# Kernel optimization log

Measured on AMD Instinct MI355X. Metric: run time of the kernel, lower is better.

The kernel has to match this reference:

```python
import jax, jax.numpy as jnp
import numpy as np
from jax import lax

B, CIN, H, W = 32, 256, 28, 28
COUT, KS, KEXP = 256, 3, 4
HIDDEN = int(CIN * 0.25)  # ratio hard-coded to 0.25 in the module


def setup_inputs() -> dict:
    key = jax.random.key(0)
    k1, k2, k3, k4 = jax.random.split(key, 4)
    x = jax.random.normal(k1, (B, CIN, H, W), dtype=jnp.float32)
    # SE (InvertedEx) params: fc1 (1x1 conv, no bias), fc2 (1x1 conv, bias)
    fc1_w = jax.random.normal(k2, (HIDDEN, CIN), dtype=jnp.float32) * np.float32(np.sqrt(2.0 / CIN))
    fc2_w = jax.random.normal(k3, (KEXP * COUT, HIDDEN), dtype=jnp.float32) * np.float32(np.sqrt(2.0 / HIDDEN))
    fc2_b = jnp.zeros((KEXP * COUT,), dtype=jnp.float32)
    # K expert conv kernels, he_std = sqrt(2) * (CIN*KS^2)^-0.5
    he_std = np.float32(np.sqrt(2.0) * (CIN * KS * KS) ** -0.5)
    weight = jax.random.normal(k4, (KEXP, COUT, CIN, KS, KS), dtype=jnp.float32) * he_std
    return {"x": x, "fc1_w": fc1_w, "fc2_w": fc2_w, "fc2_b": fc2_b, "weight": weight}


def reference(x, fc1_w, fc2_w, fc2_b, weight):
    # --- SE routing ---
    pooled = jnp.mean(x, axis=(2, 3))                        # [B, CIN]
    h = jax.nn.relu(pooled @ fc1_w.T)                        # [B, HIDDEN]
    y = (h @ fc2_w.T + fc2_b).reshape(B, KEXP, COUT)         # [B, K, COUT]
    prob = jax.nn.softmax(y / jnp.sqrt(jnp.float32(HIDDEN)), axis=1)  # softmax over K
    # --- aggregate per-sample kernels ---
    agg_w = jnp.einsum('bko,koihw->boihw', prob, weight)     # [B, COUT, CIN, KS, KS]
    # --- per-sample conv (batched implicit GEMM via vmap) ---
    def conv1(xi, wi):
        return lax.conv_general_dilated(
            xi[None], wi, window_strides=(1, 1), padding=((1, 1), (1, 1)),
            dimension_numbers=('NCHW', 'OIHW', 'NCHW'))[0]
    out = jax.vmap(conv1)(x, agg_w)                          # [B, COUT, H, W]
    return out
```

## Files before the change

### kernel.cpp

```cpp
#include <hip/hip_runtime.h>
#include <math.h>

#define B_    32
#define CIN_  256
#define HW_   784
#define H_    28
#define W_    28
#define COUT_ 256
#define KEXP_ 4
#define HID_  64

typedef short short8 __attribute__((ext_vector_type(8)));
typedef unsigned short ushort4v __attribute__((ext_vector_type(4)));
typedef float floatx16 __attribute__((ext_vector_type(16)));

__device__ __forceinline__ unsigned short f2bf(float f) {
    union { float f; unsigned int u; } v; v.f = f;
    unsigned int r = (v.u + 0x7FFFu + ((v.u >> 16) & 1u)) >> 16;
    return (unsigned short)r;
}

__global__ __launch_bounds__(256) void xpose_pool_kernel(const float* __restrict__ x,
                                                         unsigned short* __restrict__ x_t,
                                                         float* __restrict__ partial) {
    __shared__ float tile[32][33];
    int bid = blockIdx.x;
    int b   = bid / 200;
    int rem = bid - b * 200;
    int icg = rem / 25;
    int pxt = rem % 25;
    int ic0 = icg * 32;
    int px0 = pxt * 32;
    int t = threadIdx.x;
    int c = t & 31, rr = t >> 5;
    #pragma unroll
    for (int r = 0; r < 4; ++r) {
        int icr = rr + r * 8;
        int px = px0 + c;
        float v = (px < HW_) ? x[((size_t)(b * CIN_ + ic0 + icr)) * HW_ + px] : 0.f;
        tile[icr][c] = v;
    }
    __syncthreads();
    #pragma unroll
    for (int r = 0; r < 4; ++r) {
        int pxr = rr + r * 8;
        int px = px0 + pxr;
        if (px < HW_)
            x_t[((size_t)b * HW_ + px) * CIN_ + ic0 + c] = f2bf(tile[c][pxr]);
    }
    if (t < 32) {
        float s = 0.f;
        #pragma unroll
        for (int cc = 0; cc < 32; ++cc) s += tile[t][cc];
        partial[((size_t)b * 25 + pxt) * CIN_ + ic0 + t] = s * (1.0f / HW_);
    }
}

__global__ __launch_bounds__(256) void pool_kernel(const float* __restrict__ x,
                                                   float* __restrict__ pooled) {
    int w = blockIdx.x * 4 + (threadIdx.x >> 6);
    int lane = threadIdx.x & 63;
    const float* p = x + (size_t)w * HW_;
    float s = 0.f;
    for (int i = lane; i < HW_; i += 64) s += p[i];
    for (int off = 32; off; off >>= 1) s += __shfl_down(s, off);
    if (lane == 0) pooled[w] = s * (1.0f / HW_);
}

__global__ __launch_bounds__(256) void se3_kernel(const float* __restrict__ partial,
                                                  const float* __restrict__ fc1_w,
                                                  const float* __restrict__ fc2_w,
                                                  const float* __restrict__ fc2_b,
                                                  float* __restrict__ prob) {
    __shared__ float pl[CIN_];
    __shared__ float h[HID_];
    __shared__ float wb[16640];
    int b = blockIdx.x, t = threadIdx.x;
    {
        float s = 0.f;
        for (int pt = 0; pt < 25; ++pt)
            s += partial[((size_t)b * 25 + pt) * CIN_ + t];
        pl[t] = s;
    }
    #pragma unroll
    for (int i = 0; i < 16; ++i) {
        int l = t + i * 256;
        float4 v = *(const float4*)(fc1_w + (size_t)l * 4);
        int r = l >> 6, cc = (l & 63) * 4;
        float* dst = &wb[r * 257 + cc];
        dst[0] = v.x; dst[1] = v.y; dst[2] = v.z; dst[3] = v.w;
    }
    __syncthreads();
    if (t < HID_) {
        float s = 0.f;
        const float* wr = &wb[t * 257];
        for (int c = 0; c < CIN_; ++c) s += pl[c] * wr[c];
        h[t] = fmaxf(s, 0.f);
    }
    float yk[KEXP_];
    for (int k = 0; k < KEXP_; ++k) {
        __syncthreads();
        #pragma unroll
        for (int i = 0; i < 16; ++i) {
            int l = t + i * 256;
            float4 v = *(const float4*)(fc2_w + (size_t)k * COUT_ * HID_ + (size_t)l * 4);
            int o = l >> 4, jj = (l & 15) * 4;
            float* dst = &wb[o * 65 + jj];
            dst[0] = v.x; dst[1] = v.y; dst[2] = v.z; dst[3] = v.w;
        }
        __syncthreads();
        float s = fc2_b[k * COUT_ + t];
        const float* wr = &wb[t * 65];
        #pragma unroll
        for (int j = 0; j < HID_; ++j) s += h[j] * wr[j];
        yk[k] = s * 0.125f;
    }
    float m = yk[0];
    for (int k = 1; k < KEXP_; ++k) m = fmaxf(m, yk[k]);
    float e[KEXP_], sum = 0.f;
    for (int k = 0; k < KEXP_; ++k) { e[k] = expf(yk[k] - m); sum += e[k]; }
    float inv = 1.0f / sum;
    for (int k = 0; k < KEXP_; ++k)
        prob[b * (KEXP_ * COUT_) + k * COUT_ + t] = e[k] * inv;
}

__global__ __launch_bounds__(256) void se2_kernel(const float* __restrict__ pooled,
                                                  const float* __restrict__ fc1_w,
                                                  const float* __restrict__ fc2_w,
                                                  const float* __restrict__ fc2_b,
                                                  float* __restrict__ prob) {
    __shared__ float pl[CIN_];
    __shared__ float h[HID_];
    __shared__ float wb[16640];
    int b = blockIdx.x, t = threadIdx.x;
    pl[t] = pooled[b * CIN_ + t];
    #pragma unroll
    for (int i = 0; i < 16; ++i) {
        int l = t + i * 256;
        float4 v = *(const float4*)(fc1_w + (size_t)l * 4);
        int r = l >> 6, cc = (l & 63) * 4;
        float* dst = &wb[r * 257 + cc];
        dst[0] = v.x; dst[1] = v.y; dst[2] = v.z; dst[3] = v.w;
    }
    __syncthreads();
    if (t < HID_) {
        float s = 0.f;
        const float* wr = &wb[t * 257];
        for (int c = 0; c < CIN_; ++c) s += pl[c] * wr[c];
        h[t] = fmaxf(s, 0.f);
    }
    float yk[KEXP_];
    for (int k = 0; k < KEXP_; ++k) {
        __syncthreads();
        #pragma unroll
        for (int i = 0; i < 16; ++i) {
            int l = t + i * 256;
            float4 v = *(const float4*)(fc2_w + (size_t)k * COUT_ * HID_ + (size_t)l * 4);
            int o = l >> 4, jj = (l & 15) * 4;
            float* dst = &wb[o * 65 + jj];
            dst[0] = v.x; dst[1] = v.y; dst[2] = v.z; dst[3] = v.w;
        }
        __syncthreads();
        float s = fc2_b[k * COUT_ + t];
        const float* wr = &wb[t * 65];
        #pragma unroll
        for (int j = 0; j < HID_; ++j) s += h[j] * wr[j];
        yk[k] = s * 0.125f;
    }
    float m = yk[0];
    for (int k = 1; k < KEXP_; ++k) m = fmaxf(m, yk[k]);
    float e[KEXP_], sum = 0.f;
    for (int k = 0; k < KEXP_; ++k) { e[k] = expf(yk[k] - m); sum += e[k]; }
    float inv = 1.0f / sum;
    for (int k = 0; k < KEXP_; ++k)
        prob[b * (KEXP_ * COUT_) + k * COUT_ + t] = e[k] * inv;
}

__global__ __launch_bounds__(256) void agg3_kernel(const float* __restrict__ weight,
                                                   const float* __restrict__ prob,
                                                   unsigned short* __restrict__ agg) {
    __shared__ float ws_w[KEXP_ * CIN_ * 9];
    __shared__ float pb[KEXP_][8];
    int bid = blockIdx.x;
    int oc = bid & 255;
    int b0 = (bid >> 8) * 8;
    int t = threadIdx.x;
    #pragma unroll
    for (int i = 0; i < 9; ++i) {
        int e4 = t + i * 256;
        int k = e4 / 576;
        int r4 = e4 - k * 576;
        float4 v = *(const float4*)(weight + (size_t)k * 589824 + (size_t)oc * 2304 + (size_t)r4 * 4);
        *(float4*)&ws_w[e4 * 4] = v;
    }
    if (t < KEXP_ * 8) {
        int k = t >> 3, bb = t & 7;
        pb[k][bb] = prob[(size_t)(b0 + bb) * (KEXP_ * COUT_) + k * COUT_ + oc];
    }
    __syncthreads();
    int icg = t & 63, blane = t >> 6;
    for (int rs = 0; rs < 9; ++rs) {
        float wv[4][4];
        #pragma unroll
        for (int q = 0; q < 4; ++q)
            #pragma unroll
            for (int k = 0; k < 4; ++k)
                wv[q][k] = ws_w[k * 2304 + (icg * 4 + q) * 9 + rs];
        #pragma unroll
        for (int bb = 0; bb < 2; ++bb) {
            int bidx = blane * 2 + bb;
            float p0 = pb[0][bidx], p1 = pb[1][bidx], p2 = pb[2][bidx], p3 = pb[3][bidx];
            ushort4v pack;
            #pragma unroll
            for (int q = 0; q < 4; ++q) {
                float s = p0 * wv[q][0] + p1 * wv[q][1] + p2 * wv[q][2] + p3 * wv[q][3];
                pack[q] = f2bf(s);
            }
            *(ushort4v*)(agg + ((((size_t)(b0 + bidx) * 9 + rs) * COUT_ + oc)) * CIN_ + icg * 4) = pack;
        }
    }
}

__global__ __launch_bounds__(256, 1) void conv_mfma3_kernel(const unsigned short* __restrict__ x_t,
                                                            const unsigned short* __restrict__ agg,
                                                            float* __restrict__ out) {
    __shared__ __align__(16) short Xs[2][9 * 35 * 72];

    int gid = blockIdx.x;
    int b      = gid & 31;
    int oc0    = ((gid >> 5) & 1) * 128;
    int rowblk = gid >> 6;
    int py0 = rowblk * 7;

    int t = threadIdx.x;
    int lane = t & 63, w = t >> 6;
    int ml = lane & 31, kh = lane >> 5;

    floatx16 acc[7];
    #pragma unroll
    for (int j = 0; j < 7; ++j)
        #pragma unroll
        for (int r = 0; r < 16; ++r) acc[j][r] = 0.f;

    const unsigned short* xtb = x_t + (size_t)b * HW_ * CIN_;
    const unsigned short* aln = agg + (((size_t)b * 9 * COUT_) + oc0 + w * 32 + ml) * CIN_ + kh * 8;

    {
        #pragma unroll
        for (int i = 0; i < 10; ++i) {
            int l = t + i * 256;
            if (l < 2520) {
                int pos = l >> 3, g = l & 7;
                int row = pos / 35, col = pos - row * 35;
                int gy = py0 - 1 + row, gx = col - 1;
                short8 v = (short8)0;
                if ((unsigned)gy < 28u && (unsigned)gx < 28u)
                    v = *(const short8*)(xtb + ((size_t)(gy * W_ + gx)) * CIN_ + g * 8);
                *(short8*)&Xs[0][pos * 72 + g * 8] = v;
            }
        }
    }

    short8 Acur0, Acur1, Acur2, Anext0, Anext1, Anext2;
    Acur0 = *(const short8*)(aln + (size_t)(0 * 3 + 0) * (COUT_ * CIN_));
    Acur1 = *(const short8*)(aln + (size_t)(1 * 3 + 0) * (COUT_ * CIN_));
    Acur2 = *(const short8*)(aln + (size_t)(2 * 3 + 0) * (COUT_ * CIN_));
    int dxn = 1, kkn = 0, icn = 0;

    __syncthreads();

    for (int c = 0; c < 4; ++c) {
        int ic0 = c * 64;
        const short* xb = &Xs[c & 1][0];

        short8 Xl[10];
        if (c < 3) {
            #pragma unroll
            for (int i = 0; i < 10; ++i) {
                int l = t + i * 256;
                short8 v = (short8)0;
                if (l < 2520) {
                    int pos = l >> 3, g = l & 7;
                    int row = pos / 35, col = pos - row * 35;
                    int gy = py0 - 1 + row, gx = col - 1;
                    if ((unsigned)gy < 28u && (unsigned)gx < 28u)
                        v = *(const short8*)(xtb + ((size_t)(gy * W_ + gx)) * CIN_ + ic0 + 64 + g * 8);
                }
                Xl[i] = v;
            }
        }

        for (int kk = 0; kk < 4; ++kk) {
            for (int dx = 0; dx < 3; ++dx) {
                if (icn < 256) {
                    const unsigned short* ap = aln + icn + kkn * 16;
                    Anext0 = *(const short8*)(ap + (size_t)(0 * 3 + dxn) * (COUT_ * CIN_));
                    Anext1 = *(const short8*)(ap + (size_t)(1 * 3 + dxn) * (COUT_ * CIN_));
                    Anext2 = *(const short8*)(ap + (size_t)(2 * 3 + dxn) * (COUT_ * CIN_));
                    ++dxn;
                    if (dxn == 3) { dxn = 0; ++kkn; if (kkn == 4) { kkn = 0; icn += 64; } }
                }
                int va = (ml + dx) * 72 + kk * 16 + kh * 8;
                #pragma unroll
                for (int r = 0; r < 9; ++r) {
                    short8 Bf = *(const short8*)&xb[r * 2520 + va];
                    if (r <= 6)
                        acc[r]     = __builtin_amdgcn_mfma_f32_32x32x16_bf16(Acur0, Bf, acc[r], 0, 0, 0);
                    if (r >= 1 && r - 1 <= 6)
                        acc[r - 1] = __builtin_amdgcn_mfma_f32_32x32x16_bf16(Acur1, Bf, acc[r - 1], 0, 0, 0);
                    if (r >= 2)
                        acc[r - 2] = __builtin_amdgcn_mfma_f32_32x32x16_bf16(Acur2, Bf, acc[r - 2], 0, 0, 0);
                }
                Acur0 = Anext0; Acur1 = Anext1; Acur2 = Anext2;
            }
        }

        if (c < 3) {
            short* dstb = &Xs[(c & 1) ^ 1][0];
            #pragma unroll
            for (int i = 0; i < 10; ++i) {
                int l = t + i * 256;
                if (l < 2520) {
                    int pos = l >> 3, g = l & 7;
                    *(short8*)&dstb[pos * 72 + g * 8] = Xl[i];
                }
            }
        }
        __syncthreads();
    }

    if (ml < W_) {
        #pragma unroll
        for (int j = 0; j < 7; ++j) {
            float* op = out + ((size_t)(b * COUT_ + oc0 + w * 32)) * HW_ + (py0 + j) * W_ + ml;
            #pragma unroll
            for (int r = 0; r < 16; ++r) {
                int ocd = (r & 3) + 8 * (r >> 2) + 4 * kh;
                op[(size_t)ocd * HW_] = acc[j][r];
            }
        }
    }
}

__global__ __launch_bounds__(256) void conv_kernel(const float* __restrict__ x,
                                                   const float* __restrict__ weight,
                                                   const float* __restrict__ prob,
                                                   float* __restrict__ out) {
    __shared__ float xs[30 * 30];
    __shared__ float wagg[8][32][12];
    __shared__ float pl[KEXP_][8];

    int b  = blockIdx.x >> 5;
    int o0 = (blockIdx.x & 31) * 8;
    int t  = threadIdx.x;

    if (t < 32) {
        int k = t >> 3, oc = t & 7;
        pl[k][oc] = prob[b * (KEXP_ * COUT_) + k * COUT_ + o0 + oc];
    }
    int p0 = t;
    int pr[4], pc[4];
    bool pv[4];
    #pragma unroll
    for (int j = 0; j < 4; ++j) {
        int p = p0 + j * 256;
        pv[j] = p < HW_;
        pr[j] = p / W_;
        pc[j] = p % W_;
    }
    float acc[8][4];
    #pragma unroll
    for (int oc = 0; oc < 8; ++oc)
        #pragma unroll
        for (int j = 0; j < 4; ++j) acc[oc][j] = 0.f;

    int aoc = t >> 5, aii = t & 31;

    for (int ic0 = 0; ic0 < CIN_; ic0 += 32) {
        __syncthreads();
        {
            float w9[9];
            #pragma unroll
            for (int j = 0; j < 9; ++j) w9[j] = 0.f;
            int i = ic0 + aii;
            #pragma unroll
            for (int k = 0; k < KEXP_; ++k) {
                float pk = pl[k][aoc];
                const float* wp = weight + ((size_t)(k * COUT_ + o0 + aoc) * CIN_ + i) * 9;
                #pragma unroll
                for (int j = 0; j < 9; ++j) w9[j] += pk * wp[j];
            }
            #pragma unroll
            for (int j = 0; j < 9; ++j) wagg[aoc][aii][j] = w9[j];
        }
        for (int ii = 0; ii < 32; ++ii) {
            int i = ic0 + ii;
            __syncthreads();
            const float* xp = x + (size_t)(b * CIN_ + i) * HW_;
            for (int e = t; e < 900; e += 256) {
                int ry = e / 30, cx = e - ry * 30;
                int gy = ry - 1, gx = cx - 1;
                float v = 0.f;
                if ((unsigned)gy < 28u && (unsigned)gx < 28u) v = xp[gy * W_ + gx];
                xs[e] = v;
            }
            __syncthreads();
            float xv[4][9];
            #pragma unroll
            for (int j = 0; j < 4; ++j) {
                if (pv[j]) {
                    const float* xr = &xs[pr[j] * 30 + pc[j]];
                    xv[j][0] = xr[0];  xv[j][1] = xr[1];  xv[j][2] = xr[2];
                    xv[j][3] = xr[30]; xv[j][4] = xr[31]; xv[j][5] = xr[32];
                    xv[j][6] = xr[60]; xv[j][7] = xr[61]; xv[j][8] = xr[62];
                } else {
                    #pragma unroll
                    for (int q = 0; q < 9; ++q) xv[j][q] = 0.f;
                }
            }
            #pragma unroll
            for (int oc = 0; oc < 8; ++oc) {
                float4 wa = *(const float4*)&wagg[oc][ii][0];
                float4 wb2 = *(const float4*)&wagg[oc][ii][4];
                float  wc = wagg[oc][ii][8];
                #pragma unroll
                for (int j = 0; j < 4; ++j) {
                    acc[oc][j] += xv[j][0] * wa.x + xv[j][1] * wa.y + xv[j][2] * wa.z
                                + xv[j][3] * wa.w + xv[j][4] * wb2.x + xv[j][5] * wb2.y
                                + xv[j][6] * wb2.z + xv[j][7] * wb2.w + xv[j][8] * wc;
                }
            }
        }
    }
    #pragma unroll
    for (int oc = 0; oc < 8; ++oc) {
        float* op = out + (size_t)(b * COUT_ + o0 + oc) * HW_ + p0;
        #pragma unroll
        for (int j = 0; j < 4; ++j)
            if (pv[j]) op[j * 256] = acc[oc][j];
    }
}

extern "C" void kernel_launch(void* const* d_in, const int* in_sizes, int n_in,
                              void* d_out, int out_size, void* d_ws, size_t ws_size,
                              hipStream_t stream) {
    const float* x     = (const float*)d_in[0];
    const float* fc1_w = (const float*)d_in[1];
    const float* fc2_w = (const float*)d_in[2];
    const float* fc2_b = (const float*)d_in[3];
    const float* weight= (const float*)d_in[4];
    float* out = (float*)d_out;

    char* ws = (char*)d_ws;
    float* prob = (float*)(ws);
    unsigned short* x_t = (unsigned short*)(ws + 131072);
    unsigned short* agg = (unsigned short*)(ws + 12976128);
    float* partial = (float*)(ws + 12976128);
    const size_t WS_NEED = 12976128 + (size_t)B_ * 9 * COUT_ * CIN_ * 2;

    if (ws_size >= WS_NEED) {
        xpose_pool_kernel<<<B_ * 8 * 25, 256, 0, stream>>>(x, x_t, partial);
        se3_kernel<<<B_, 256, 0, stream>>>(partial, fc1_w, fc2_w, fc2_b, prob);
        agg3_kernel<<<4 * COUT_, 256, 0, stream>>>(weight, prob, agg);
        conv_mfma3_kernel<<<256, 256, 0, stream>>>(x_t, agg, out);
    } else {
        float* pooled = (float*)(ws + 131072);
        pool_kernel<<<(B_ * CIN_) / 4, 256, 0, stream>>>(x, pooled);
        se2_kernel<<<B_, 256, 0, stream>>>(pooled, fc1_w, fc2_w, fc2_b, prob);
        conv_kernel<<<B_ * (COUT_ / 8), 256, 0, stream>>>(x, weight, prob, out);
    }
}
```

Before: 149.9 us.

## Fuse routing, aggregation and conv into one cooperative persistent kernel

Merges the transpose/pool, SE, kernel aggregation and MFMA conv stages into one cooperative kernel of 512 blocks, separated by grid-wide syncs, so the separate kernel launches and their gaps go away. The conv is retiled from 7 output rows per block to 4 (448 blocks, two blocks per CU), and each aggregation block now handles 16 samples instead of 8. If the cooperative launch fails, the same stages run as separate kernels. The trade-off is grid-sync cost, idle blocks during the SE stage, and load imbalance from 448 conv blocks on 512 slots. The old small-workspace fallback path is also removed.

```diff
diff --git a/kernel.cpp b/kernel.cpp
--- a/kernel.cpp
+++ b/kernel.cpp
@@ -1,5 +1,8 @@
 #include <hip/hip_runtime.h>
+#include <hip/hip_cooperative_groups.h>
 #include <math.h>
+
+namespace cg = cooperative_groups;
 
 #define B_    32
 #define CIN_  256
@@ -10,6 +13,8 @@
 #define KEXP_ 4
 #define HID_  64
 
+#define SMEM_BYTES 67840
+
 typedef short short8 __attribute__((ext_vector_type(8)));
 typedef unsigned short ushort4v __attribute__((ext_vector_type(4)));
 typedef float floatx16 __attribute__((ext_vector_type(16)));
@@ -20,18 +25,17 @@
     return (unsigned short)r;
 }
 
-__global__ __launch_bounds__(256) void xpose_pool_kernel(const float* __restrict__ x,
-                                                         unsigned short* __restrict__ x_t,
-                                                         float* __restrict__ partial) {
-    __shared__ float tile[32][33];
-    int bid = blockIdx.x;
+__device__ __forceinline__ void do_xpose_unit(const float* __restrict__ x,
+                                              unsigned short* __restrict__ x_t,
+                                              float* __restrict__ partial,
+                                              char* sm, int bid, int t) {
+    float (*tile)[33] = (float (*)[33])sm;
     int b   = bid / 200;
     int rem = bid - b * 200;
     int icg = rem / 25;
     int pxt = rem % 25;
     int ic0 = icg * 32;
     int px0 = pxt * 32;
-    int t = threadIdx.x;
     int c = t & 31, rr = t >> 5;
     #pragma unroll
     for (int r = 0; r < 4; ++r) {
@@ -54,28 +58,18 @@
         for (int cc = 0; cc < 32; ++cc) s += tile[t][cc];
         partial[((size_t)b * 25 + pxt) * CIN_ + ic0 + t] = s * (1.0f / HW_);
     }
-}
-
-__global__ __launch_bounds__(256) void pool_kernel(const float* __restrict__ x,
-                                                   float* __restrict__ pooled) {
-    int w = blockIdx.x * 4 + (threadIdx.x >> 6);
-    int lane = threadIdx.x & 63;
-    const float* p = x + (size_t)w * HW_;
-    float s = 0.f;
-    for (int i = lane; i < HW_; i += 64) s += p[i];
-    for (int off = 32; off; off >>= 1) s += __shfl_down(s, off);
-    if (lane == 0) pooled[w] = s * (1.0f / HW_);
-}
-
-__global__ __launch_bounds__(256) void se3_kernel(const float* __restrict__ partial,
-                                                  const float* __restrict__ fc1_w,
-                                                  const float* __restrict__ fc2_w,
-                                                  const float* __restrict__ fc2_b,
-                                                  float* __restrict__ prob) {
-    __shared__ float pl[CIN_];
-    __shared__ float h[HID_];
-    __shared__ float wb[16640];
-    int b = blockIdx.x, t = threadIdx.x;
+    __syncthreads();
+}
+
+__device__ __forceinline__ void do_se(const float* __restrict__ partial,
+                                      const float* __restrict__ fc1_w,
+                                      const float* __restrict__ fc2_w,
+                                      const float* __restrict__ fc2_b,
+                                      float* __restrict__ prob,
+                                      char* sm, int b, int t) {
+    float* pl = (float*)sm;
+    float* h  = pl + 256;
+    float* wb = h + 64;
     {
         float s = 0.f;
         for (int pt = 0; pt < 25; ++pt)
@@ -124,67 +118,12 @@
         prob[b * (KEXP_ * COUT_) + k * COUT_ + t] = e[k] * inv;
 }
 
-__global__ __launch_bounds__(256) void se2_kernel(const float* __restrict__ pooled,
-                                                  const float* __restrict__ fc1_w,
-                                                  const float* __restrict__ fc2_w,
-                                                  const float* __restrict__ fc2_b,
-                                                  float* __restrict__ prob) {
-    __shared__ float pl[CIN_];
-    __shared__ float h[HID_];
-    __shared__ float wb[16640];
-    int b = blockIdx.x, t = threadIdx.x;
-    pl[t] = pooled[b * CIN_ + t];
-    #pragma unroll
-    for (int i = 0; i < 16; ++i) {
-        int l = t + i * 256;
-        float4 v = *(const float4*)(fc1_w + (size_t)l * 4);
-        int r = l >> 6, cc = (l & 63) * 4;
-        float* dst = &wb[r * 257 + cc];
-        dst[0] = v.x; dst[1] = v.y; dst[2] = v.z; dst[3] = v.w;
-    }
-    __syncthreads();
-    if (t < HID_) {
-        float s = 0.f;
-        const float* wr = &wb[t * 257];
-        for (int c = 0; c < CIN_; ++c) s += pl[c] * wr[c];
-        h[t] = fmaxf(s, 0.f);
-    }
-    float yk[KEXP_];
-    for (int k = 0; k < KEXP_; ++k) {
-        __syncthreads();
-        #pragma unroll
-        for (int i = 0; i < 16; ++i) {
-            int l = t + i * 256;
-            float4 v = *(const float4*)(fc2_w + (size_t)k * COUT_ * HID_ + (size_t)l * 4);
-            int o = l >> 4, jj = (l & 15) * 4;
-            float* dst = &wb[o * 65 + jj];
-            dst[0] = v.x; dst[1] = v.y; dst[2] = v.z; dst[3] = v.w;
-        }
-        __syncthreads();
-        float s = fc2_b[k * COUT_ + t];
-        const float* wr = &wb[t * 65];
-        #pragma unroll
-        for (int j = 0; j < HID_; ++j) s += h[j] * wr[j];
-        yk[k] = s * 0.125f;
-    }
-    float m = yk[0];
-    for (int k = 1; k < KEXP_; ++k) m = fmaxf(m, yk[k]);
-    float e[KEXP_], sum = 0.f;
-    for (int k = 0; k < KEXP_; ++k) { e[k] = expf(yk[k] - m); sum += e[k]; }
-    float inv = 1.0f / sum;
-    for (int k = 0; k < KEXP_; ++k)
-        prob[b * (KEXP_ * COUT_) + k * COUT_ + t] = e[k] * inv;
-}
-
-__global__ __launch_bounds__(256) void agg3_kernel(const float* __restrict__ weight,
-                                                   const float* __restrict__ prob,
-                                                   unsigned short* __restrict__ agg) {
-    __shared__ float ws_w[KEXP_ * CIN_ * 9];
-    __shared__ float pb[KEXP_][8];
-    int bid = blockIdx.x;
-    int oc = bid & 255;
-    int b0 = (bid >> 8) * 8;
-    int t = threadIdx.x;
+__device__ __forceinline__ void do_agg_unit(const float* __restrict__ weight,
+                                            const float* __restrict__ prob,
+                                            unsigned short* __restrict__ agg,
+                                            char* sm, int oc, int b0, int t) {
+    float* ws_w = (float*)sm;
+    float* pb   = ws_w + 9216;
     #pragma unroll
     for (int i = 0; i < 9; ++i) {
         int e4 = t + i * 256;
@@ -193,9 +132,9 @@
         float4 v = *(const float4*)(weight + (size_t)k * 589824 + (size_t)oc * 2304 + (size_t)r4 * 4);
         *(float4*)&ws_w[e4 * 4] = v;
     }
-    if (t < KEXP_ * 8) {
-        int k = t >> 3, bb = t & 7;
-        pb[k][bb] = prob[(size_t)(b0 + bb) * (KEXP_ * COUT_) + k * COUT_ + oc];
+    if (t < 64) {
+        int k = t >> 4, bb = t & 15;
+        pb[k * 16 + bb] = prob[(size_t)(b0 + bb) * (KEXP_ * COUT_) + k * COUT_ + oc];
     }
     __syncthreads();
     int icg = t & 63, blane = t >> 6;
@@ -207,79 +146,80 @@
             for (int k = 0; k < 4; ++k)
                 wv[q][k] = ws_w[k * 2304 + (icg * 4 + q) * 9 + rs];
         #pragma unroll
-        for (int bb = 0; bb < 2; ++bb) {
-            int bidx = blane * 2 + bb;
-            float p0 = pb[0][bidx], p1 = pb[1][bidx], p2 = pb[2][bidx], p3 = pb[3][bidx];
+        for (int bb = 0; bb < 4; ++bb) {
+            int bidx = blane * 4 + bb;
+            float p0 = pb[0 * 16 + bidx], p1 = pb[1 * 16 + bidx];
+            float p2 = pb[2 * 16 + bidx], p3 = pb[3 * 16 + bidx];
             ushort4v pack;
             #pragma unroll
             for (int q = 0; q < 4; ++q) {
                 float s = p0 * wv[q][0] + p1 * wv[q][1] + p2 * wv[q][2] + p3 * wv[q][3];
                 pack[q] = f2bf(s);
             }
-            *(ushort4v*)(agg + ((((size_t)(b0 + bidx) * 9 + rs) * COUT_ + oc)) * CIN_ + icg * 4) = pack;
-        }
-    }
-}
-
-__global__ __launch_bounds__(256, 1) void conv_mfma3_kernel(const unsigned short* __restrict__ x_t,
-                                                            const unsigned short* __restrict__ agg,
-                                                            float* __restrict__ out) {
-    __shared__ __align__(16) short Xs[2][9 * 35 * 72];
-
-    int gid = blockIdx.x;
+            *(ushort4v*)(agg + (((size_t)(b0 + bidx) * 9 + rs) * COUT_ + oc) * CIN_ + icg * 4) = pack;
+        }
+    }
+    __syncthreads();
+}
+
+__device__ void do_conv(const unsigned short* __restrict__ x_t,
+                        const unsigned short* __restrict__ agg,
+                        float* __restrict__ out,
+                        char* sm, int gid, int t) {
+    short* Xs0 = (short*)sm;
+    short* Xs1 = Xs0 + 15120;
+
     int b      = gid & 31;
     int oc0    = ((gid >> 5) & 1) * 128;
     int rowblk = gid >> 6;
-    int py0 = rowblk * 7;
-
-    int t = threadIdx.x;
+    int py0 = rowblk * 4;
+
     int lane = t & 63, w = t >> 6;
     int ml = lane & 31, kh = lane >> 5;
 
-    floatx16 acc[7];
-    #pragma unroll
-    for (int j = 0; j < 7; ++j)
+    floatx16 acc[4];
+    #pragma unroll
+    for (int j = 0; j < 4; ++j)
         #pragma unroll
         for (int r = 0; r < 16; ++r) acc[j][r] = 0.f;
 
     const unsigned short* xtb = x_t + (size_t)b * HW_ * CIN_;
     const unsigned short* aln = agg + (((size_t)b * 9 * COUT_) + oc0 + w * 32 + ml) * CIN_ + kh * 8;
 
-    {
-        #pragma unroll
-        for (int i = 0; i < 10; ++i) {
-            int l = t + i * 256;
-            if (l < 2520) {
-                int pos = l >> 3, g = l & 7;
-                int row = pos / 35, col = pos - row * 35;
-                int gy = py0 - 1 + row, gx = col - 1;
-                short8 v = (short8)0;
-                if ((unsigned)gy < 28u && (unsigned)gx < 28u)
-                    v = *(const short8*)(xtb + ((size_t)(gy * W_ + gx)) * CIN_ + g * 8);
-                *(short8*)&Xs[0][pos * 72 + g * 8] = v;
-            }
+    #pragma unroll
+    for (int i = 0; i < 7; ++i) {
+        int l = t + i * 256;
+        if (l < 1680) {
+            int pos = l >> 3, g = l & 7;
+            int row = pos / 35, col = pos - row * 35;
+            int gy = py0 - 1 + row, gx = col - 1;
+            short8 v = (short8)0;
+            if ((unsigned)gy < 28u && (unsigned)gx < 28u)
+                v = *(const short8*)(xtb + ((size_t)(gy * W_ + gx)) * CIN_ + g * 8);
+            *(short8*)&Xs0[pos * 72 + g * 8] = v;
         }
     }
 
     short8 Acur0, Acur1, Acur2, Anext0, Anext1, Anext2;
-    Acur0 = *(const short8*)(aln + (size_t)(0 * 3 + 0) * (COUT_ * CIN_));
-    Acur1 = *(const short8*)(aln + (size_t)(1 * 3 + 0) * (COUT_ * CIN_));
-    Acur2 = *(const short8*)(aln + (size_t)(2 * 3 + 0) * (COUT_ * CIN_));
+    Acur0 = *(const short8*)(aln + (size_t)0 * (COUT_ * CIN_));
+    Acur1 = *(const short8*)(aln + (size_t)3 * (COUT_ * CIN_));
+    Acur2 = *(const short8*)(aln + (size_t)6 * (COUT_ * CIN_));
     int dxn = 1, kkn = 0, icn = 0;
 
     __syncthreads();
 
     for (int c = 0; c < 4; ++c) {
         int ic0 = c * 64;
-        const short* xb = &Xs[c & 1][0];
-
-        short8 Xl[10];
+        const short* xb = (c & 1) ? Xs1 : Xs0;
+        short*       xo = (c & 1) ? Xs0 : Xs1;
+
+        short8 Xl[7];
         if (c < 3) {
             #pragma unroll
-            for (int i = 0; i < 10; ++i) {
+            for (int i = 0; i < 7; ++i) {
                 int l = t + i * 256;
                 short8 v = (short8)0;
-                if (l < 2520) {
+                if (l < 1680) {
                     int pos = l >> 3, g = l & 7;
                     int row = pos / 35, col = pos - row * 35;
                     int gy = py0 - 1 + row, gx = col - 1;
@@ -302,11 +242,11 @@
                 }
                 int va = (ml + dx) * 72 + kk * 16 + kh * 8;
                 #pragma unroll
-                for (int r = 0; r < 9; ++r) {
+                for (int r = 0; r < 6; ++r) {
                     short8 Bf = *(const short8*)&xb[r * 2520 + va];
-                    if (r <= 6)
+                    if (r <= 3)
                         acc[r]     = __builtin_amdgcn_mfma_f32_32x32x16_bf16(Acur0, Bf, acc[r], 0, 0, 0);
-                    if (r >= 1 && r - 1 <= 6)
+                    if (r >= 1 && r <= 4)
                         acc[r - 1] = __builtin_amdgcn_mfma_f32_32x32x16_bf16(Acur1, Bf, acc[r - 1], 0, 0, 0);
                     if (r >= 2)
                         acc[r - 2] = __builtin_amdgcn_mfma_f32_32x32x16_bf16(Acur2, Bf, acc[r - 2], 0, 0, 0);
@@ -316,13 +256,12 @@
         }
 
         if (c < 3) {
-            short* dstb = &Xs[(c & 1) ^ 1][0];
-            #pragma unroll
-            for (int i = 0; i < 10; ++i) {
+            #pragma unroll
+            for (int i = 0; i < 7; ++i) {
                 int l = t + i * 256;
-                if (l < 2520) {
+                if (l < 1680) {
                     int pos = l >> 3, g = l & 7;
-                    *(short8*)&dstb[pos * 72 + g * 8] = Xl[i];
+                    *(short8*)&xo[pos * 72 + g * 8] = Xl[i];
                 }
             }
         }
@@ -331,7 +270,7 @@
 
     if (ml < W_) {
         #pragma unroll
-        for (int j = 0; j < 7; ++j) {
+        for (int j = 0; j < 4; ++j) {
             float* op = out + ((size_t)(b * COUT_ + oc0 + w * 32)) * HW_ + (py0 + j) * W_ + ml;
             #pragma unroll
             for (int r = 0; r < 16; ++r) {
@@ -342,103 +281,63 @@
     }
 }
 
-__global__ __launch_bounds__(256) void conv_kernel(const float* __restrict__ x,
-                                                   const float* __restrict__ weight,
-                                                   const float* __restrict__ prob,
-                                                   float* __restrict__ out) {
-    __shared__ float xs[30 * 30];
-    __shared__ float wagg[8][32][12];
-    __shared__ float pl[KEXP_][8];
-
-    int b  = blockIdx.x >> 5;
-    int o0 = (blockIdx.x & 31) * 8;
-    int t  = threadIdx.x;
-
-    if (t < 32) {
-        int k = t >> 3, oc = t & 7;
-        pl[k][oc] = prob[b * (KEXP_ * COUT_) + k * COUT_ + o0 + oc];
-    }
-    int p0 = t;
-    int pr[4], pc[4];
-    bool pv[4];
-    #pragma unroll
-    for (int j = 0; j < 4; ++j) {
-        int p = p0 + j * 256;
-        pv[j] = p < HW_;
-        pr[j] = p / W_;
-        pc[j] = p % W_;
-    }
-    float acc[8][4];
-    #pragma unroll
-    for (int oc = 0; oc < 8; ++oc)
-        #pragma unroll
-        for (int j = 0; j < 4; ++j) acc[oc][j] = 0.f;
-
-    int aoc = t >> 5, aii = t & 31;
-
-    for (int ic0 = 0; ic0 < CIN_; ic0 += 32) {
-        __syncthreads();
-        {
-            float w9[9];
-            #pragma unroll
-            for (int j = 0; j < 9; ++j) w9[j] = 0.f;
-            int i = ic0 + aii;
-            #pragma unroll
-            for (int k = 0; k < KEXP_; ++k) {
-                float pk = pl[k][aoc];
-                const float* wp = weight + ((size_t)(k * COUT_ + o0 + aoc) * CIN_ + i) * 9;
-                #pragma unroll
-                for (int j = 0; j < 9; ++j) w9[j] += pk * wp[j];
-            }
-            #pragma unroll
-            for (int j = 0; j < 9; ++j) wagg[aoc][aii][j] = w9[j];
-        }
-        for (int ii = 0; ii < 32; ++ii) {
-            int i = ic0 + ii;
-            __syncthreads();
-            const float* xp = x + (size_t)(b * CIN_ + i) * HW_;
-            for (int e = t; e < 900; e += 256) {
-                int ry = e / 30, cx = e - ry * 30;
-                int gy = ry - 1, gx = cx - 1;
-                float v = 0.f;
-                if ((unsigned)gy < 28u && (unsigned)gx < 28u) v = xp[gy * W_ + gx];
-                xs[e] = v;
-            }
-            __syncthreads();
-            float xv[4][9];
-            #pragma unroll
-            for (int j = 0; j < 4; ++j) {
-                if (pv[j]) {
-                    const float* xr = &xs[pr[j] * 30 + pc[j]];
-                    xv[j][0] = xr[0];  xv[j][1] = xr[1];  xv[j][2] = xr[2];
-                    xv[j][3] = xr[30]; xv[j][4] = xr[31]; xv[j][5] = xr[32];
-                    xv[j][6] = xr[60]; xv[j][7] = xr[61]; xv[j][8] = xr[62];
-                } else {
-                    #pragma unroll
-                    for (int q = 0; q < 9; ++q) xv[j][q] = 0.f;
-                }
-            }
-            #pragma unroll
-            for (int oc = 0; oc < 8; ++oc) {
-                float4 wa = *(const float4*)&wagg[oc][ii][0];
-                float4 wb2 = *(const float4*)&wagg[oc][ii][4];
-                float  wc = wagg[oc][ii][8];
-                #pragma unroll
-                for (int j = 0; j < 4; ++j) {
-                    acc[oc][j] += xv[j][0] * wa.x + xv[j][1] * wa.y + xv[j][2] * wa.z
-                                + xv[j][3] * wa.w + xv[j][4] * wb2.x + xv[j][5] * wb2.y
-                                + xv[j][6] * wb2.z + xv[j][7] * wb2.w + xv[j][8] * wc;
-                }
-            }
-        }
-    }
-    #pragma unroll
-    for (int oc = 0; oc < 8; ++oc) {
-        float* op = out + (size_t)(b * COUT_ + o0 + oc) * HW_ + p0;
-        #pragma unroll
-        for (int j = 0; j < 4; ++j)
-            if (pv[j]) op[j * 256] = acc[oc][j];
-    }
+__global__ void __launch_bounds__(256, 2) fused_kernel(const float* __restrict__ x,
+                                                       const float* __restrict__ fc1_w,
+                                                       const float* __restrict__ fc2_w,
+                                                       const float* __restrict__ fc2_b,
+                                                       const float* __restrict__ weight,
+                                                       unsigned short* __restrict__ x_t,
+                                                       unsigned short* __restrict__ agg,
+                                                       float* __restrict__ partial,
+                                                       float* __restrict__ prob,
+                                                       float* __restrict__ out) {
+    __shared__ __align__(16) char sm[SMEM_BYTES];
+    cg::grid_group grid = cg::this_grid();
+    int g = blockIdx.x, t = threadIdx.x;
+
+    for (int i = 0; i < 13; ++i) {
+        int bid = g + 512 * i;
+        if (bid < 6400) do_xpose_unit(x, x_t, partial, sm, bid, t);
+    }
+    __threadfence();
+    grid.sync();
+
+    if (g < 32) do_se(partial, fc1_w, fc2_w, fc2_b, prob, sm, g, t);
+    __threadfence();
+    grid.sync();
+
+    do_agg_unit(weight, prob, agg, sm, g & 255, (g >> 8) * 16, t);
+    __threadfence();
+    grid.sync();
+
+    if (g < 448) do_conv(x_t, agg, out, sm, g, t);
+}
+
+__global__ __launch_bounds__(256) void k_xpose(const float* __restrict__ x,
+                                               unsigned short* __restrict__ x_t,
+                                               float* __restrict__ partial) {
+    __shared__ __align__(16) char sm[4224];
+    do_xpose_unit(x, x_t, partial, sm, blockIdx.x, threadIdx.x);
+}
+__global__ __launch_bounds__(256) void k_se(const float* __restrict__ partial,
+                                            const float* __restrict__ fc1_w,
+                                            const float* __restrict__ fc2_w,
+                                            const float* __restrict__ fc2_b,
+                                            float* __restrict__ prob) {
+    __shared__ __align__(16) char sm[67840];
+    do_se(partial, fc1_w, fc2_w, fc2_b, prob, sm, blockIdx.x, threadIdx.x);
+}
+__global__ __launch_bounds__(256) void k_agg(const float* __restrict__ weight,
+                                             const float* __restrict__ prob,
+                                             unsigned short* __restrict__ agg) {
+    __shared__ __align__(16) char sm[37120];
+    do_agg_unit(weight, prob, agg, sm, blockIdx.x & 255, (blockIdx.x >> 8) * 16, threadIdx.x);
+}
+__global__ __launch_bounds__(256, 2) void k_conv(const unsigned short* __restrict__ x_t,
+                                                 const unsigned short* __restrict__ agg,
+                                                 float* __restrict__ out) {
+    __shared__ __align__(16) char sm[60480];
+    do_conv(x_t, agg, out, sm, blockIdx.x, threadIdx.x);
 }
 
 extern "C" void kernel_launch(void* const* d_in, const int* in_sizes, int n_in,
@@ -456,17 +355,15 @@
     unsigned short* x_t = (unsigned short*)(ws + 131072);
     unsigned short* agg = (unsigned short*)(ws + 12976128);
     float* partial = (float*)(ws + 12976128);
-    const size_t WS_NEED = 12976128 + (size_t)B_ * 9 * COUT_ * CIN_ * 2;
-
-    if (ws_size >= WS_NEED) {
-        xpose_pool_kernel<<<B_ * 8 * 25, 256, 0, stream>>>(x, x_t, partial);
-        se3_kernel<<<B_, 256, 0, stream>>>(partial, fc1_w, fc2_w, fc2_b, prob);
-        agg3_kernel<<<4 * COUT_, 256, 0, stream>>>(weight, prob, agg);
-        conv_mfma3_kernel<<<256, 256, 0, stream>>>(x_t, agg, out);
-    } else {
-        float* pooled = (float*)(ws + 131072);
-        pool_kernel<<<(B_ * CIN_) / 4, 256, 0, stream>>>(x, pooled);
-        se2_kernel<<<B_, 256, 0, stream>>>(pooled, fc1_w, fc2_w, fc2_b, prob);
-        conv_kernel<<<B_ * (COUT_ / 8), 256, 0, stream>>>(x, weight, prob, out);
-    }
-}
+
+    void* args[] = {(void*)&x, (void*)&fc1_w, (void*)&fc2_w, (void*)&fc2_b, (void*)&weight,
+                    (void*)&x_t, (void*)&agg, (void*)&partial, (void*)&prob, (void*)&out};
+    hipError_t err = hipLaunchCooperativeKernel((const void*)fused_kernel,
+                                                dim3(512), dim3(256), args, 0, stream);
+    if (err != hipSuccess) {
+        k_xpose<<<6400, 256, 0, stream>>>(x, x_t, partial);
+        k_se<<<32, 256, 0, stream>>>(partial, fc1_w, fc2_w, fc2_b, prob);
+        k_agg<<<512, 256, 0, stream>>>(weight, prob, agg);
+        k_conv<<<448, 256, 0, stream>>>(x_t, agg, out);
+    }
+}
```

New measurement: 437.3 us. 192% more time.

## Shrink conv row tile to 4 rows for more blocks and occupancy, single-buffer LDS

Applied to the files above, without the earlier changes.

The MFMA conv kernel now computes 4 output rows per block instead of 7, giving 448 blocks instead of 256. It drops the register-staged double buffer for a single LDS buffer of 6 halo rows, with launch bounds raised to allow 3 blocks per CU. The aggregation kernel also handles 16 batches per block instead of 8, launching half as many blocks. The aim is better CU coverage and overlap across co-resident blocks, at the cost of more halo reloads and exposed global-load latency inside each block.

```diff
diff --git a/kernel.cpp b/kernel.cpp
--- a/kernel.cpp
+++ b/kernel.cpp
@@ -176,14 +176,14 @@
         prob[b * (KEXP_ * COUT_) + k * COUT_ + t] = e[k] * inv;
 }
 
-__global__ __launch_bounds__(256) void agg3_kernel(const float* __restrict__ weight,
+__global__ __launch_bounds__(256) void agg4_kernel(const float* __restrict__ weight,
                                                    const float* __restrict__ prob,
                                                    unsigned short* __restrict__ agg) {
     __shared__ float ws_w[KEXP_ * CIN_ * 9];
-    __shared__ float pb[KEXP_][8];
+    __shared__ float pb[KEXP_][16];
     int bid = blockIdx.x;
     int oc = bid & 255;
-    int b0 = (bid >> 8) * 8;
+    int b0 = (bid >> 8) * 16;
     int t = threadIdx.x;
     #pragma unroll
     for (int i = 0; i < 9; ++i) {
@@ -193,8 +193,8 @@
         float4 v = *(const float4*)(weight + (size_t)k * 589824 + (size_t)oc * 2304 + (size_t)r4 * 4);
         *(float4*)&ws_w[e4 * 4] = v;
     }
-    if (t < KEXP_ * 8) {
-        int k = t >> 3, bb = t & 7;
+    if (t < 64) {
+        int k = t >> 4, bb = t & 15;
         pb[k][bb] = prob[(size_t)(b0 + bb) * (KEXP_ * COUT_) + k * COUT_ + oc];
     }
     __syncthreads();
@@ -207,8 +207,8 @@
             for (int k = 0; k < 4; ++k)
                 wv[q][k] = ws_w[k * 2304 + (icg * 4 + q) * 9 + rs];
         #pragma unroll
-        for (int bb = 0; bb < 2; ++bb) {
-            int bidx = blane * 2 + bb;
+        for (int bb = 0; bb < 4; ++bb) {
+            int bidx = blane * 4 + bb;
             float p0 = pb[0][bidx], p1 = pb[1][bidx], p2 = pb[2][bidx], p3 = pb[3][bidx];
             ushort4v pack;
             #pragma unroll
@@ -216,79 +216,57 @@
                 float s = p0 * wv[q][0] + p1 * wv[q][1] + p2 * wv[q][2] + p3 * wv[q][3];
                 pack[q] = f2bf(s);
             }
-            *(ushort4v*)(agg + ((((size_t)(b0 + bidx) * 9 + rs) * COUT_ + oc)) * CIN_ + icg * 4) = pack;
-        }
-    }
-}
-
-__global__ __launch_bounds__(256, 1) void conv_mfma3_kernel(const unsigned short* __restrict__ x_t,
+            *(ushort4v*)(agg + (((size_t)(b0 + bidx) * 9 + rs) * COUT_ + oc) * CIN_ + icg * 4) = pack;
+        }
+    }
+}
+
+__global__ __launch_bounds__(256, 3) void conv_mfma4_kernel(const unsigned short* __restrict__ x_t,
                                                             const unsigned short* __restrict__ agg,
                                                             float* __restrict__ out) {
-    __shared__ __align__(16) short Xs[2][9 * 35 * 72];
+    __shared__ __align__(16) short Xs[6 * 35 * 72];
 
     int gid = blockIdx.x;
     int b      = gid & 31;
     int oc0    = ((gid >> 5) & 1) * 128;
     int rowblk = gid >> 6;
-    int py0 = rowblk * 7;
+    int py0 = rowblk * 4;
 
     int t = threadIdx.x;
     int lane = t & 63, w = t >> 6;
     int ml = lane & 31, kh = lane >> 5;
 
-    floatx16 acc[7];
-    #pragma unroll
-    for (int j = 0; j < 7; ++j)
+    floatx16 acc[4];
+    #pragma unroll
+    for (int j = 0; j < 4; ++j)
         #pragma unroll
         for (int r = 0; r < 16; ++r) acc[j][r] = 0.f;
 
     const unsigned short* xtb = x_t + (size_t)b * HW_ * CIN_;
     const unsigned short* aln = agg + (((size_t)b * 9 * COUT_) + oc0 + w * 32 + ml) * CIN_ + kh * 8;
 
-    {
-        #pragma unroll
-        for (int i = 0; i < 10; ++i) {
+    short8 Acur0, Acur1, Acur2, Anext0, Anext1, Anext2;
+    Acur0 = *(const short8*)(aln + (size_t)0 * (COUT_ * CIN_));
+    Acur1 = *(const short8*)(aln + (size_t)3 * (COUT_ * CIN_));
+    Acur2 = *(const short8*)(aln + (size_t)6 * (COUT_ * CIN_));
+    int dxn = 1, kkn = 0, icn = 0;
+
+    for (int c = 0; c < 4; ++c) {
+        if (c) __syncthreads();
+        #pragma unroll
+        for (int i = 0; i < 7; ++i) {
             int l = t + i * 256;
-            if (l < 2520) {
+            if (l < 1680) {
                 int pos = l >> 3, g = l & 7;
                 int row = pos / 35, col = pos - row * 35;
                 int gy = py0 - 1 + row, gx = col - 1;
                 short8 v = (short8)0;
                 if ((unsigned)gy < 28u && (unsigned)gx < 28u)
-                    v = *(const short8*)(xtb + ((size_t)(gy * W_ + gx)) * CIN_ + g * 8);
-                *(short8*)&Xs[0][pos * 72 + g * 8] = v;
-            }
-        }
-    }
-
-    short8 Acur0, Acur1, Acur2, Anext0, Anext1, Anext2;
-    Acur0 = *(const short8*)(aln + (size_t)(0 * 3 + 0) * (COUT_ * CIN_));
-    Acur1 = *(const short8*)(aln + (size_t)(1 * 3 + 0) * (COUT_ * CIN_));
-    Acur2 = *(const short8*)(aln + (size_t)(2 * 3 + 0) * (COUT_ * CIN_));
-    int dxn = 1, kkn = 0, icn = 0;
-
-    __syncthreads();
-
-    for (int c = 0; c < 4; ++c) {
-        int ic0 = c * 64;
-        const short* xb = &Xs[c & 1][0];
-
-        short8 Xl[10];
-        if (c < 3) {
-            #pragma unroll
-            for (int i = 0; i < 10; ++i) {
-                int l = t + i * 256;
-                short8 v = (short8)0;
-                if (l < 2520) {
-                    int pos = l >> 3, g = l & 7;
-                    int row = pos / 35, col = pos - row * 35;
-                    int gy = py0 - 1 + row, gx = col - 1;
-                    if ((unsigned)gy < 28u && (unsigned)gx < 28u)
-                        v = *(const short8*)(xtb + ((size_t)(gy * W_ + gx)) * CIN_ + ic0 + 64 + g * 8);
-                }
-                Xl[i] = v;
-            }
-        }
+                    v = *(const short8*)(xtb + ((size_t)(gy * W_ + gx)) * CIN_ + c * 64 + g * 8);
+                *(short8*)&Xs[pos * 72 + g * 8] = v;
+            }
+        }
+        __syncthreads();
 
         for (int kk = 0; kk < 4; ++kk) {
             for (int dx = 0; dx < 3; ++dx) {
@@ -302,11 +280,11 @@
                 }
                 int va = (ml + dx) * 72 + kk * 16 + kh * 8;
                 #pragma unroll
-                for (int r = 0; r < 9; ++r) {
-                    short8 Bf = *(const short8*)&xb[r * 2520 + va];
-                    if (r <= 6)
+                for (int r = 0; r < 6; ++r) {
+                    short8 Bf = *(const short8*)&Xs[r * 2520 + va];
+                    if (r <= 3)
                         acc[r]     = __builtin_amdgcn_mfma_f32_32x32x16_bf16(Acur0, Bf, acc[r], 0, 0, 0);
-                    if (r >= 1 && r - 1 <= 6)
+                    if (r >= 1 && r <= 4)
                         acc[r - 1] = __builtin_amdgcn_mfma_f32_32x32x16_bf16(Acur1, Bf, acc[r - 1], 0, 0, 0);
                     if (r >= 2)
                         acc[r - 2] = __builtin_amdgcn_mfma_f32_32x32x16_bf16(Acur2, Bf, acc[r - 2], 0, 0, 0);
@@ -314,24 +292,11 @@
                 Acur0 = Anext0; Acur1 = Anext1; Acur2 = Anext2;
             }
         }
-
-        if (c < 3) {
-            short* dstb = &Xs[(c & 1) ^ 1][0];
-            #pragma unroll
-            for (int i = 0; i < 10; ++i) {
-                int l = t + i * 256;
-                if (l < 2520) {
-                    int pos = l >> 3, g = l & 7;
-                    *(short8*)&dstb[pos * 72 + g * 8] = Xl[i];
-                }
-            }
-        }
-        __syncthreads();
     }
 
     if (ml < W_) {
         #pragma unroll
-        for (int j = 0; j < 7; ++j) {
+        for (int j = 0; j < 4; ++j) {
             float* op = out + ((size_t)(b * COUT_ + oc0 + w * 32)) * HW_ + (py0 + j) * W_ + ml;
             #pragma unroll
             for (int r = 0; r < 16; ++r) {
@@ -461,8 +426,8 @@
     if (ws_size >= WS_NEED) {
         xpose_pool_kernel<<<B_ * 8 * 25, 256, 0, stream>>>(x, x_t, partial);
         se3_kernel<<<B_, 256, 0, stream>>>(partial, fc1_w, fc2_w, fc2_b, prob);
-        agg3_kernel<<<4 * COUT_, 256, 0, stream>>>(weight, prob, agg);
-        conv_mfma3_kernel<<<256, 256, 0, stream>>>(x_t, agg, out);
+        agg4_kernel<<<512, 256, 0, stream>>>(weight, prob, agg);
+        conv_mfma4_kernel<<<448, 256, 0, stream>>>(x_t, agg, out);
     } else {
         float* pooled = (float*)(ws + 131072);
         pool_kernel<<<(B_ * CIN_) / 4, 256, 0, stream>>>(x, pooled);
```

Result: slower. 158.7 us (+5.9%).
